# Kernel tuning notes

Measured on AMD Instinct MI355X. Metric: run time of the kernel, lower is better.

## Reference

```python
import jax, jax.numpy as jnp
import numpy as np
from jax import lax

K = 3      # kernel_size
G = 2      # group
EPS = 1e-5 # BatchNorm eps


def setup_inputs() -> dict:
    key = jax.random.key(0)
    k1, k2 = jax.random.split(key)
    y = jax.random.normal(k1, (4, 64, 256, 256), dtype=jnp.float32)
    # kaiming-normal fan_out init for conv weight (18, 64, 3, 3)
    fan_out = 18 * K * K
    std = np.sqrt(2.0 / fan_out)
    w_conv = jax.random.normal(k2, (G * K * K, 64, K, K), dtype=jnp.float32) * std
    gamma = jnp.ones((G * K * K,), dtype=jnp.float32)
    beta = jnp.zeros((G * K * K,), dtype=jnp.float32)
    return {"y": y, "w_conv": w_conv, "gamma": gamma, "beta": beta}


def reference(y, w_conv, gamma, beta):
    N, C, H, W = y.shape
    pad = K // 2
    # reflect-pad so conv and unfold keep H, W (required by the h*w reshape)
    yp = jnp.pad(y, ((0, 0), (0, 0), (pad, pad), (pad, pad)), mode="reflect")

    # sigma = softmax(BN(conv(y))) over the G*K*K channel dim
    sigma = lax.conv_general_dilated(
        yp, w_conv, window_strides=(1, 1), padding="VALID",
        dimension_numbers=("NCHW", "OIHW", "NCHW"))  # (N, G*K*K, H, W)
    mean = jnp.mean(sigma, axis=(0, 2, 3), keepdims=True)
    var = jnp.var(sigma, axis=(0, 2, 3), keepdims=True)  # biased, as torch BN train
    sigma = (sigma - mean) * lax.rsqrt(var + EPS)
    sigma = sigma * gamma[None, :, None, None] + beta[None, :, None, None]
    sigma = jax.nn.softmax(sigma, axis=1)

    # unfold: (N, C, K*K, H, W) with row-major kernel-window ordering (matches F.unfold)
    patches = jnp.stack(
        [yp[:, :, i:i + H, j:j + W] for i in range(K) for j in range(K)], axis=2)
    patches = patches.reshape(N, G, C // G, K * K, H * W)  # group-major channel split
    sig = sigma.reshape(N, G, K * K, H * W)                # group-major split of G*K*K

    # per-pixel dynamic conv: weighted sum over the K*K window positions
    out = jnp.einsum("ngckq,ngkq->ngcq", patches, sig).reshape(N, C, H, W)
    v_map = sig[:, :, None, :, :]  # (N, G, 1, K*K, H*W), as in the torch code
    return out, v_map
```

## Files before the change

kernel.cpp:

```cpp
#include <hip/hip_runtime.h>

#define NB 4
#define CB 64
#define HB 256
#define WB 256
#define OB 18
#define HWB (HB*WB)
#define TILE 16
#define ICC 8
#define EPSV 1e-5f

__device__ __forceinline__ int reflect_idx(int i, int n) {
    if (i < 0) i = -i;
    if (i >= n) i = 2*n - 2 - i;
    return i;
}

__device__ __forceinline__ void ldsdma4(const float* g, float* l) {
    __builtin_amdgcn_global_load_lds(
        (__attribute__((address_space(1))) unsigned int*)g,
        (__attribute__((address_space(3))) unsigned int*)l, 4, 0, 0);
}

__global__ __launch_bounds__(256) void transpose_w_kernel(
    const float* __restrict__ w, float* __restrict__ wt)
{
    int i = blockIdx.x * 256 + threadIdx.x;
    if (i < OB*CB*9) {
        int o   = i / (CB*9);
        int rem = i - o*CB*9;
        int c   = rem / 9;
        int k   = rem - c*9;
        wt[c*OB*9 + o*9 + k] = w[i];
    }
}

#define STAGE(dst, cb) do {                                            \
    const float* _yb = ybase + (size_t)(cb)*HWB;                       \
    _Pragma("unroll")                                                  \
    for (int _i = 0; _i < 10; ++_i)                                    \
        ldsdma4(_yb + sofs[_i], (dst) + tid + _i*256);                 \
    if (tid < 32) ldsdma4(_yb + sofs[10], (dst) + tid + 2560);         \
} while (0)

__global__ __launch_bounds__(256) void conv_stats_kernel(
    const float* __restrict__ y, const float* __restrict__ wt,
    float* __restrict__ sigma, float* __restrict__ psum, float* __restrict__ psq)
{
    __shared__ float tile[2][ICC*324];
    __shared__ float red[4][36];
    const int tid = threadIdx.x;
    const int tx = tid & 15, ty = tid >> 4;
    const int bx = blockIdx.x, by = blockIdx.y, n = blockIdx.z;
    const int h0 = by * TILE, w0 = bx * TILE;

    int sofs[11];
#pragma unroll
    for (int i = 0; i < 11; ++i) {
        int j  = tid + i*256;
        int jj = (j < ICC*324) ? j : 0;
        int c   = jj / 324;
        int rem = jj - c*324;
        int r   = rem / 18;
        int col = rem - r*18;
        sofs[i] = c*HWB + reflect_idx(h0 - 1 + r, HB)*WB + reflect_idx(w0 - 1 + col, WB);
    }

    const float* ybase = y + (size_t)n*CB*HWB;

    float acc[OB];
#pragma unroll
    for (int o = 0; o < OB; ++o) acc[o] = 0.f;

    STAGE(tile[0], 0);
    __syncthreads();

    int cur = 0;
    for (int cb = 0; cb < CB; cb += ICC) {
        if (cb + ICC < CB) STAGE(tile[cur^1], cb + ICC);
        const float* tl = tile[cur];
#pragma unroll
        for (int ii = 0; ii < ICC; ++ii) {
            float v[9];
#pragma unroll
            for (int dy = 0; dy < 3; ++dy)
#pragma unroll
                for (int dx = 0; dx < 3; ++dx)
                    v[dy*3+dx] = tl[ii*324 + (ty+dy)*18 + tx+dx];
            const float* wp = wt + (cb + ii)*162;
#pragma unroll
            for (int o = 0; o < OB; ++o)
#pragma unroll
                for (int k = 0; k < 9; ++k)
                    acc[o] = fmaf(v[k], wp[o*9 + k], acc[o]);
        }
        __syncthreads();
        cur ^= 1;
    }

    const int q = (h0 + ty)*WB + (w0 + tx);
#pragma unroll
    for (int o = 0; o < OB; ++o)
        sigma[((size_t)n*OB + o)*HWB + q] = acc[o];

    const int lane = tid & 63, wv = tid >> 6;
#pragma unroll
    for (int o = 0; o < OB; ++o) {
        float s  = acc[o];
        float s2 = acc[o]*acc[o];
        for (int off = 32; off > 0; off >>= 1) {
            s  += __shfl_down(s,  off, 64);
            s2 += __shfl_down(s2, off, 64);
        }
        if (lane == 0) { red[wv][o] = s; red[wv][o + OB] = s2; }
    }
    __syncthreads();
    if (tid < 36) {
        float t = red[0][tid] + red[1][tid] + red[2][tid] + red[3][tid];
        const int bid = (n*16 + by)*16 + bx;
        if (tid < OB) psum[tid*1024 + bid] = t;
        else          psq[(tid-OB)*1024 + bid] = t;
    }
}

__global__ __launch_bounds__(256) void stats_kernel(
    const float* __restrict__ psum, const float* __restrict__ psq,
    const float* __restrict__ gamma, const float* __restrict__ beta,
    float* __restrict__ scale, float* __restrict__ shift)
{
    const int o = blockIdx.x;
    const int t = threadIdx.x;
    float s = 0.f, s2 = 0.f;
#pragma unroll
    for (int i = 0; i < 4; ++i) {
        s  += psum[o*1024 + t + i*256];
        s2 += psq [o*1024 + t + i*256];
    }
    for (int off = 32; off > 0; off >>= 1) {
        s  += __shfl_down(s,  off, 64);
        s2 += __shfl_down(s2, off, 64);
    }
    __shared__ float red[8];
    const int lane = t & 63, wv = t >> 6;
    if (lane == 0) { red[wv] = s; red[wv + 4] = s2; }
    __syncthreads();
    if (t == 0) {
        float S  = red[0] + red[1] + red[2] + red[3];
        float SS = red[4] + red[5] + red[6] + red[7];
        const float cnt = (float)(NB * HWB);
        float mean = S / cnt;
        float var  = SS / cnt - mean*mean;
        float sc = gamma[o] * rsqrtf(var + EPSV);
        scale[o] = sc;
        shift[o] = beta[o] - mean * sc;
    }
}

__global__ __launch_bounds__(256) void softmax_apply_kernel(
    const float* __restrict__ y, const float* __restrict__ sigma,
    const float* __restrict__ scale, const float* __restrict__ shift,
    float* __restrict__ out)
{
    __shared__ float tile[2][ICC*324];
    const int tid = threadIdx.x;
    const int tx = tid & 15, ty = tid >> 4;
    const int bx = blockIdx.x, by = blockIdx.y, n = blockIdx.z;
    const int h0 = by * TILE, w0 = bx * TILE;
    const int q = (h0 + ty)*WB + (w0 + tx);

    int sofs[11];
#pragma unroll
    for (int i = 0; i < 11; ++i) {
        int j  = tid + i*256;
        int jj = (j < ICC*324) ? j : 0;
        int c   = jj / 324;
        int rem = jj - c*324;
        int r   = rem / 18;
        int col = rem - r*18;
        sofs[i] = c*HWB + reflect_idx(h0 - 1 + r, HB)*WB + reflect_idx(w0 - 1 + col, WB);
    }

    const float* ybase = y + (size_t)n*CB*HWB;

    STAGE(tile[0], 0);

    float z[OB];
#pragma unroll
    for (int o = 0; o < OB; ++o)
        z[o] = fmaf(sigma[((size_t)n*OB + o)*HWB + q], scale[o], shift[o]);

    float m = z[0];
#pragma unroll
    for (int o = 1; o < OB; ++o) m = fmaxf(m, z[o]);
    float sum = 0.f;
#pragma unroll
    for (int o = 0; o < OB; ++o) { z[o] = __expf(z[o] - m); sum += z[o]; }
    const float r = 1.f / sum;

    float* vmap = out + (size_t)NB*CB*HWB;
#pragma unroll
    for (int o = 0; o < OB; ++o) {
        z[o] *= r;
        vmap[((size_t)n*OB + o)*HWB + q] = z[o];
    }

    float* obase = out + (size_t)n*CB*HWB;
    __syncthreads();

#pragma unroll
    for (int ci = 0; ci < 8; ++ci) {
        const int cb = ci * ICC;
        if (ci < 7) STAGE(tile[(ci&1)^1], cb + ICC);
        const float* tl = tile[ci&1];
#pragma unroll
        for (int ii = 0; ii < ICC; ++ii) {
            float a = 0.f;
#pragma unroll
            for (int dy = 0; dy < 3; ++dy)
#pragma unroll
                for (int dx = 0; dx < 3; ++dx)
                    a = fmaf(tl[ii*324 + (ty+dy)*18 + tx+dx], z[(cb>>5)*9 + dy*3 + dx], a);
            obase[(size_t)(cb + ii)*HWB + q] = a;
        }
        __syncthreads();
    }
}

extern "C" void kernel_launch(void* const* d_in, const int* in_sizes, int n_in,
                              void* d_out, int out_size, void* d_ws, size_t ws_size,
                              hipStream_t stream) {
    const float* y     = (const float*)d_in[0];
    const float* w     = (const float*)d_in[1];
    const float* gamma = (const float*)d_in[2];
    const float* beta  = (const float*)d_in[3];
    float* out = (float*)d_out;

    float* sigma = (float*)d_ws;
    float* wt    = sigma + (size_t)NB*OB*HWB;
    float* psum  = wt + OB*CB*9;
    float* psq   = psum + OB*1024;
    float* scale = psq  + OB*1024;
    float* shift = scale + OB;

    dim3 grid(WB/TILE, HB/TILE, NB);
    dim3 block(256);
    transpose_w_kernel<<<dim3((OB*CB*9 + 255)/256), block, 0, stream>>>(w, wt);
    conv_stats_kernel<<<grid, block, 0, stream>>>(y, wt, sigma, psum, psq);
    stats_kernel<<<dim3(OB), block, 0, stream>>>(psum, psq, gamma, beta, scale, shift);
    softmax_apply_kernel<<<grid, block, 0, stream>>>(y, sigma, scale, shift, out);
}
```

Measured before the change: 308.5 us.

## Register-block conv over 4 pixels per thread and split output channels across waves

The conv kernel now has each thread compute 4 adjacent pixels of one row, and each wave handles a subset of 4 or 5 output channels instead of all 18. LDS reads become float2 and are reused across the 4 pixels. Stores become float4, and block statistics are written directly per wave without the shared reduction. The apply kernel is remapped the same way: each thread handles 4 pixels and each wave 2 channels per chunk, with vectorized sigma, vmap and output accesses. The aim is to cut LDS traffic and global transactions per FMA, at the cost of more registers per thread and uneven work across waves.

```diff
diff --git a/kernel.cpp b/kernel.cpp
--- a/kernel.cpp
+++ b/kernel.cpp
@@ -43,14 +43,27 @@
     if (tid < 32) ldsdma4(_yb + sofs[10], (dst) + tid + 2560);         \
 } while (0)
 
+#define LOADV(tl, ii) do {                                             \
+    _Pragma("unroll")                                                  \
+    for (int _dy = 0; _dy < 3; ++_dy) {                                \
+        const float2* _t2 = (const float2*)((tl) + (ii)*324 + (r+_dy)*18 + c0); \
+        float2 _a = _t2[0], _b = _t2[1], _c = _t2[2];                  \
+        v[_dy][0]=_a.x; v[_dy][1]=_a.y; v[_dy][2]=_b.x;                \
+        v[_dy][3]=_b.y; v[_dy][4]=_c.x; v[_dy][5]=_c.y;                \
+    }                                                                  \
+} while (0)
+
 __global__ __launch_bounds__(256) void conv_stats_kernel(
     const float* __restrict__ y, const float* __restrict__ wt,
     float* __restrict__ sigma, float* __restrict__ psum, float* __restrict__ psq)
 {
     __shared__ float tile[2][ICC*324];
-    __shared__ float red[4][36];
     const int tid = threadIdx.x;
-    const int tx = tid & 15, ty = tid >> 4;
+    const int lane = tid & 63, wv = tid >> 6;
+    const int r  = lane >> 2;
+    const int c0 = (lane & 3) * 4;
+    const int o0 = (wv < 2) ? wv*5 : wv*4 + 2;
+    const bool has5 = (wv < 2);
     const int bx = blockIdx.x, by = blockIdx.y, n = blockIdx.z;
     const int h0 = by * TILE, w0 = bx * TILE;
 
@@ -61,16 +74,18 @@
         int jj = (j < ICC*324) ? j : 0;
         int c   = jj / 324;
         int rem = jj - c*324;
-        int r   = rem / 18;
-        int col = rem - r*18;
-        sofs[i] = c*HWB + reflect_idx(h0 - 1 + r, HB)*WB + reflect_idx(w0 - 1 + col, WB);
+        int rr  = rem / 18;
+        int col = rem - rr*18;
+        sofs[i] = c*HWB + reflect_idx(h0 - 1 + rr, HB)*WB + reflect_idx(w0 - 1 + col, WB);
     }
 
     const float* ybase = y + (size_t)n*CB*HWB;
 
-    float acc[OB];
-#pragma unroll
-    for (int o = 0; o < OB; ++o) acc[o] = 0.f;
+    float acc[4][5];
+#pragma unroll
+    for (int j = 0; j < 4; ++j)
+#pragma unroll
+        for (int oi = 0; oi < 5; ++oi) acc[j][oi] = 0.f;
 
     STAGE(tile[0], 0);
     __syncthreads();
@@ -81,45 +96,51 @@
         const float* tl = tile[cur];
 #pragma unroll
         for (int ii = 0; ii < ICC; ++ii) {
-            float v[9];
-#pragma unroll
-            for (int dy = 0; dy < 3; ++dy)
-#pragma unroll
-                for (int dx = 0; dx < 3; ++dx)
-                    v[dy*3+dx] = tl[ii*324 + (ty+dy)*18 + tx+dx];
-            const float* wp = wt + (cb + ii)*162;
-#pragma unroll
-            for (int o = 0; o < OB; ++o)
-#pragma unroll
-                for (int k = 0; k < 9; ++k)
-                    acc[o] = fmaf(v[k], wp[o*9 + k], acc[o]);
+            float v[3][6];
+            LOADV(tl, ii);
+            const float* wp = wt + (cb + ii)*162 + o0*9;
+#pragma unroll
+            for (int oi = 0; oi < 4; ++oi)
+#pragma unroll
+                for (int dy = 0; dy < 3; ++dy)
+#pragma unroll
+                    for (int dx = 0; dx < 3; ++dx) {
+                        const float w_ = wp[oi*9 + dy*3 + dx];
+#pragma unroll
+                        for (int j = 0; j < 4; ++j)
+                            acc[j][oi] = fmaf(v[dy][dx+j], w_, acc[j][oi]);
+                    }
+            if (has5)
+#pragma unroll
+                for (int dy = 0; dy < 3; ++dy)
+#pragma unroll
+                    for (int dx = 0; dx < 3; ++dx) {
+                        const float w_ = wp[36 + dy*3 + dx];
+#pragma unroll
+                        for (int j = 0; j < 4; ++j)
+                            acc[j][4] = fmaf(v[dy][dx+j], w_, acc[j][4]);
+                    }
         }
         __syncthreads();
         cur ^= 1;
     }
 
-    const int q = (h0 + ty)*WB + (w0 + tx);
-#pragma unroll
-    for (int o = 0; o < OB; ++o)
-        sigma[((size_t)n*OB + o)*HWB + q] = acc[o];
-
-    const int lane = tid & 63, wv = tid >> 6;
-#pragma unroll
-    for (int o = 0; o < OB; ++o) {
-        float s  = acc[o];
-        float s2 = acc[o]*acc[o];
+    const int qbase = (h0 + r)*WB + w0 + c0;
+    const int bid = (n*16 + by)*16 + bx;
+#pragma unroll
+    for (int oi = 0; oi < 5; ++oi) {
+        if (oi == 4 && !has5) break;
+        const int o = o0 + oi;
+        *(float4*)(sigma + ((size_t)n*OB + o)*HWB + qbase) =
+            make_float4(acc[0][oi], acc[1][oi], acc[2][oi], acc[3][oi]);
+        float s  = acc[0][oi] + acc[1][oi] + acc[2][oi] + acc[3][oi];
+        float s2 = acc[0][oi]*acc[0][oi] + acc[1][oi]*acc[1][oi]
+                 + acc[2][oi]*acc[2][oi] + acc[3][oi]*acc[3][oi];
         for (int off = 32; off > 0; off >>= 1) {
             s  += __shfl_down(s,  off, 64);
             s2 += __shfl_down(s2, off, 64);
         }
-        if (lane == 0) { red[wv][o] = s; red[wv][o + OB] = s2; }
-    }
-    __syncthreads();
-    if (tid < 36) {
-        float t = red[0][tid] + red[1][tid] + red[2][tid] + red[3][tid];
-        const int bid = (n*16 + by)*16 + bx;
-        if (tid < OB) psum[tid*1024 + bid] = t;
-        else          psq[(tid-OB)*1024 + bid] = t;
+        if (lane == 0) { psum[o*1024 + bid] = s; psq[o*1024 + bid] = s2; }
     }
 }
 
@@ -163,10 +184,12 @@
 {
     __shared__ float tile[2][ICC*324];
     const int tid = threadIdx.x;
-    const int tx = tid & 15, ty = tid >> 4;
+    const int lane = tid & 63, wv = tid >> 6;
+    const int r  = lane >> 2;
+    const int c0 = (lane & 3) * 4;
     const int bx = blockIdx.x, by = blockIdx.y, n = blockIdx.z;
     const int h0 = by * TILE, w0 = bx * TILE;
-    const int q = (h0 + ty)*WB + (w0 + tx);
+    const int qbase = (h0 + r)*WB + w0 + c0;
 
     int sofs[11];
 #pragma unroll
@@ -175,34 +198,43 @@
         int jj = (j < ICC*324) ? j : 0;
         int c   = jj / 324;
         int rem = jj - c*324;
-        int r   = rem / 18;
-        int col = rem - r*18;
-        sofs[i] = c*HWB + reflect_idx(h0 - 1 + r, HB)*WB + reflect_idx(w0 - 1 + col, WB);
+        int rr  = rem / 18;
+        int col = rem - rr*18;
+        sofs[i] = c*HWB + reflect_idx(h0 - 1 + rr, HB)*WB + reflect_idx(w0 - 1 + col, WB);
     }
 
     const float* ybase = y + (size_t)n*CB*HWB;
 
     STAGE(tile[0], 0);
 
-    float z[OB];
+    float z[4][18];
+#pragma unroll
+    for (int o = 0; o < OB; ++o) {
+        const float4 sg = *(const float4*)(sigma + ((size_t)n*OB + o)*HWB + qbase);
+        const float sc = scale[o], sh = shift[o];
+        z[0][o] = fmaf(sg.x, sc, sh);
+        z[1][o] = fmaf(sg.y, sc, sh);
+        z[2][o] = fmaf(sg.z, sc, sh);
+        z[3][o] = fmaf(sg.w, sc, sh);
+    }
+#pragma unroll
+    for (int j = 0; j < 4; ++j) {
+        float m = z[j][0];
+#pragma unroll
+        for (int o = 1; o < OB; ++o) m = fmaxf(m, z[j][o]);
+        float sum = 0.f;
+#pragma unroll
+        for (int o = 0; o < OB; ++o) { z[j][o] = __expf(z[j][o] - m); sum += z[j][o]; }
+        const float rs = 1.f / sum;
+#pragma unroll
+        for (int o = 0; o < OB; ++o) z[j][o] *= rs;
+    }
+
+    float* vmap = out + (size_t)NB*CB*HWB;
 #pragma unroll
     for (int o = 0; o < OB; ++o)
-        z[o] = fmaf(sigma[((size_t)n*OB + o)*HWB + q], scale[o], shift[o]);
-
-    float m = z[0];
-#pragma unroll
-    for (int o = 1; o < OB; ++o) m = fmaxf(m, z[o]);
-    float sum = 0.f;
-#pragma unroll
-    for (int o = 0; o < OB; ++o) { z[o] = __expf(z[o] - m); sum += z[o]; }
-    const float r = 1.f / sum;
-
-    float* vmap = out + (size_t)NB*CB*HWB;
-#pragma unroll
-    for (int o = 0; o < OB; ++o) {
-        z[o] *= r;
-        vmap[((size_t)n*OB + o)*HWB + q] = z[o];
-    }
+        *(float4*)(vmap + ((size_t)n*OB + o)*HWB + qbase) =
+            make_float4(z[0][o], z[1][o], z[2][o], z[3][o]);
 
     float* obase = out + (size_t)n*CB*HWB;
     __syncthreads();
@@ -212,15 +244,25 @@
         const int cb = ci * ICC;
         if (ci < 7) STAGE(tile[(ci&1)^1], cb + ICC);
         const float* tl = tile[ci&1];
-#pragma unroll
-        for (int ii = 0; ii < ICC; ++ii) {
-            float a = 0.f;
+        const int g = ci >> 2;
+#pragma unroll
+        for (int jj = 0; jj < 2; ++jj) {
+            const int ii = 2*wv + jj;
+            float v[3][6];
+            LOADV(tl, ii);
+            float a0 = 0.f, a1 = 0.f, a2 = 0.f, a3 = 0.f;
 #pragma unroll
             for (int dy = 0; dy < 3; ++dy)
 #pragma unroll
-                for (int dx = 0; dx < 3; ++dx)
-                    a = fmaf(tl[ii*324 + (ty+dy)*18 + tx+dx], z[(cb>>5)*9 + dy*3 + dx], a);
-            obase[(size_t)(cb + ii)*HWB + q] = a;
+                for (int dx = 0; dx < 3; ++dx) {
+                    const int k = g*9 + dy*3 + dx;
+                    a0 = fmaf(v[dy][dx+0], z[0][k], a0);
+                    a1 = fmaf(v[dy][dx+1], z[1][k], a1);
+                    a2 = fmaf(v[dy][dx+2], z[2][k], a2);
+                    a3 = fmaf(v[dy][dx+3], z[3][k], a3);
+                }
+            *(float4*)(obase + (size_t)(cb + ii)*HWB + qbase) =
+                make_float4(a0, a1, a2, a3);
         }
         __syncthreads();
     }
```

Measured after the change: 532.8 us. +72.7%, slower.
